# Kernel tuning notes

Measured on AMD Instinct MI355X. Metric: run time of the kernel, lower is better.

## Reference

```python
import jax, jax.numpy as jnp
import numpy as np

DIM = 256
NUM_HEADS = 8
HEAD_DIM = DIM // NUM_HEADS
NUM_MAIN = 2
NUM_MOD = 4
SEQ_MAIN = 1536
SEQ_AUX = 768
BS = 2


def setup_inputs() -> dict:
    key = jax.random.key(0)
    ks = jax.random.split(key, 6)
    x0 = jax.random.normal(ks[0], (BS, SEQ_MAIN, DIM), jnp.float32)
    x1 = jax.random.normal(ks[1], (BS, SEQ_MAIN, DIM), jnp.float32)
    x2 = jax.random.normal(ks[2], (BS, SEQ_AUX, DIM), jnp.float32)
    x3 = jax.random.normal(ks[3], (BS, SEQ_AUX, DIM), jnp.float32)
    Wqkv = jax.random.normal(ks[4], (NUM_MOD, DIM, 3 * DIM), jnp.float32) * 0.02
    bqkv = jnp.zeros((NUM_MOD, 3 * DIM), jnp.float32)
    Wproj = jax.random.normal(ks[5], (NUM_MOD, DIM, DIM), jnp.float32) * 0.02
    bproj = jnp.zeros((NUM_MOD, DIM), jnp.float32)
    return {"x0": x0, "x1": x1, "x2": x2, "x3": x3,
            "Wqkv": Wqkv, "bqkv": bqkv, "Wproj": Wproj, "bproj": bproj}


def _split_qkv(qkv):
    bs, s, _ = qkv.shape
    qkv = qkv.reshape(bs, s, 3, NUM_HEADS, HEAD_DIM).transpose(2, 0, 3, 1, 4)
    return qkv[0], qkv[1], qkv[2]


def _sdpa(q, k, v):
    scale = 1.0 / jnp.sqrt(jnp.asarray(HEAD_DIM, q.dtype))
    scores = jnp.einsum('bhqd,bhkd->bhqk', q, k) * scale
    probs = jax.nn.softmax(scores, axis=-1)
    return jnp.einsum('bhqk,bhkd->bhqd', probs, v)


def _merge_heads(t):
    # [bs, heads, s, head_dim] -> [bs, s, dim]
    bs, h, s, d = t.shape
    return t.transpose(0, 2, 1, 3).reshape(bs, s, h * d)


def reference(x0, x1, x2, x3, Wqkv, bqkv, Wproj, bproj):
    xs = [x0, x1, x2, x3]
    seqlens = [x.shape[1] for x in xs]
    qs, ks, vs = [], [], []
    for i in range(NUM_MOD):
        q, k, v = _split_qkv(xs[i] @ Wqkv[i] + bqkv[i])
        qs.append(q); ks.append(k); vs.append(v)

    main_q = jnp.concatenate(qs[:NUM_MAIN], axis=2)
    main_k = jnp.concatenate(ks[:NUM_MAIN], axis=2)
    main_v = jnp.concatenate(vs[:NUM_MAIN], axis=2)
    main_x = _merge_heads(_sdpa(main_q, main_k, main_v))  # [bs, sum(main seqlens), dim]
    splits = np.cumsum(seqlens[:NUM_MAIN])[:-1]
    outs = list(jnp.split(main_x, splits, axis=1))

    # aux modalities attend over detached main KV + own KV
    mk = jax.lax.stop_gradient(main_k)
    mv = jax.lax.stop_gradient(main_v)
    for i in range(NUM_MAIN, NUM_MOD):
        k = jnp.concatenate([mk, ks[i]], axis=2)
        v = jnp.concatenate([mv, vs[i]], axis=2)
        outs.append(_merge_heads(_sdpa(qs[i], k, v)))

    outs = [outs[i] @ Wproj[i] + bproj[i] for i in range(NUM_MOD)]
    # concatenate per-modality outputs along the sequence dim for a single output
    return jnp.concatenate(outs, axis=1)
```

## Files before the change

### kernel.cpp

```cpp
#include <hip/hip_runtime.h>
#include <hip/hip_bf16.h>
#include <math.h>

#define BS 2
#define NHEADS 8
#define HD 32
#define DIM 256
#define W3 768
#define S_MAIN 1536
#define S_AUX 768
#define SM_TOT 3072
#define S_TOT 4608

typedef _Float16 f16x8 __attribute__((ext_vector_type(8)));
typedef _Float16 f16x4 __attribute__((ext_vector_type(4)));
typedef float    f32x4 __attribute__((ext_vector_type(4)));

#define QK_SCALE 0.25503491f

#define QM_H  0
#define KM_H  1572864
#define VMT_H 3145728
#define QA_H  4718592
#define KA_H  5505024
#define VAT_H 6291456
#define AO0_F 3538944
#define AO1_F 5898240
#define L0_F  8257536
#define L1_F  8266752

#define GLOAD_LDS(SRC, DST)                                                    \
    __builtin_amdgcn_global_load_lds(                                          \
        (const __attribute__((address_space(1))) void*)(SRC),                  \
        (__attribute__((address_space(3))) void*)(DST), 16, 0, 0)

__global__ __launch_bounds__(256) void qkv_mfma_kernel(
    const float* __restrict__ x0, const float* __restrict__ x1,
    const float* __restrict__ x2, const float* __restrict__ x3,
    const float* __restrict__ Wqkv, const float* __restrict__ bqkv,
    _Float16* __restrict__ wsh)
{
    const int m  = blockIdx.z;
    const int rt = blockIdx.y;
    const int ct = blockIdx.x;
    const int s_m   = (m < 2) ? S_MAIN : S_AUX;
    const int nrows = BS * s_m;
    const int r0 = rt * 128;
    if (r0 >= nrows) return;

    const float* x    = (m == 0) ? x0 : (m == 1) ? x1 : (m == 2) ? x2 : x3;
    const float* W    = Wqkv + m * (DIM * W3);
    const float* bias = bqkv + m * W3;

    __shared__ _Float16 As[128][40];
    __shared__ _Float16 Bs[64][40];

    const int t    = threadIdx.x;
    const int wid  = t >> 6;
    const int lane = t & 63;
    const int g    = lane >> 4;
    const int c    = lane & 15;
    const int c0   = ct * 64;

    const int arow = t >> 1;
    const int ak   = (t & 1) << 4;
    const int bcol = t & 63;
    const int bkg  = t >> 6;
    const int bsg  = bkg ^ ((bcol >> 3) & 3);

    f32x4 acc[2][4];
    #pragma unroll
    for (int i = 0; i < 2; ++i)
        #pragma unroll
        for (int j = 0; j < 4; ++j)
            acc[i][j] = (f32x4){0.f, 0.f, 0.f, 0.f};

    const float* xp = x + (r0 + arow) * DIM + ak;
    const float* wp = W + (bkg * 8) * W3 + c0 + bcol;

    for (int kk = 0; kk < DIM; kk += 32) {
        {
            const float4 u0 = *(const float4*)(xp + kk + 0);
            const float4 u1 = *(const float4*)(xp + kk + 4);
            const float4 u2 = *(const float4*)(xp + kk + 8);
            const float4 u3 = *(const float4*)(xp + kk + 12);
            f16x8 h0, h1;
            h0[0] = (_Float16)u0.x; h0[1] = (_Float16)u0.y;
            h0[2] = (_Float16)u0.z; h0[3] = (_Float16)u0.w;
            h0[4] = (_Float16)u1.x; h0[5] = (_Float16)u1.y;
            h0[6] = (_Float16)u1.z; h0[7] = (_Float16)u1.w;
            h1[0] = (_Float16)u2.x; h1[1] = (_Float16)u2.y;
            h1[2] = (_Float16)u2.z; h1[3] = (_Float16)u2.w;
            h1[4] = (_Float16)u3.x; h1[5] = (_Float16)u3.y;
            h1[6] = (_Float16)u3.z; h1[7] = (_Float16)u3.w;
            *(f16x8*)&As[arow][ak]     = h0;
            *(f16x8*)&As[arow][ak + 8] = h1;
        }
        {
            const float* wq = wp + kk * W3;
            f16x8 hb;
            hb[0] = (_Float16)wq[0 * W3]; hb[1] = (_Float16)wq[1 * W3];
            hb[2] = (_Float16)wq[2 * W3]; hb[3] = (_Float16)wq[3 * W3];
            hb[4] = (_Float16)wq[4 * W3]; hb[5] = (_Float16)wq[5 * W3];
            hb[6] = (_Float16)wq[6 * W3]; hb[7] = (_Float16)wq[7 * W3];
            *(f16x8*)&Bs[bcol][bsg << 3] = hb;
        }
        __syncthreads();
        const f16x8 af0 = *(const f16x8*)&As[wid * 32 + c][g * 8];
        const f16x8 af1 = *(const f16x8*)&As[wid * 32 + 16 + c][g * 8];
        #pragma unroll
        for (int j = 0; j < 4; ++j) {
            const int bc = j * 16 + c;
            const int gg = g ^ ((bc >> 3) & 3);
            const f16x8 bf = *(const f16x8*)&Bs[bc][gg * 8];
            acc[0][j] = __builtin_amdgcn_mfma_f32_16x16x32_f16(af0, bf, acc[0][j], 0, 0, 0);
            acc[1][j] = __builtin_amdgcn_mfma_f32_16x16x32_f16(af1, bf, acc[1][j], 0, 0, 0);
        }
        __syncthreads();
    }

    #pragma unroll
    for (int i = 0; i < 2; ++i) {
        const int gr = r0 + wid * 32 + i * 16 + 4 * g;
        const int b  = (gr >= s_m) ? 1 : 0;
        const int s  = gr - (b ? s_m : 0);
        #pragma unroll
        for (int j = 0; j < 4; ++j) {
            const int col   = c0 + j * 16 + c;
            const int which = col >> 8;
            const int head  = (col >> 5) & 7;
            const int dd    = col & 31;
            const float bv  = bias[col];
            const f32x4 a   = acc[i][j];
            if (which < 2) {
                const float qs = (which == 0) ? QK_SCALE : 1.0f;
                _Float16* dst;
                int base;
                if (m < 2) {
                    dst  = wsh + (which == 0 ? QM_H : KM_H);
                    base = ((b * NHEADS + head) * SM_TOT + (s + m * S_MAIN)) * HD + dd;
                } else {
                    dst  = wsh + (which == 0 ? QA_H : KA_H);
                    base = ((((m - 2) * BS + b) * NHEADS + head) * S_AUX + s) * HD + dd;
                }
                dst[base + 0 * HD] = (_Float16)((a[0] + bv) * qs);
                dst[base + 1 * HD] = (_Float16)((a[1] + bv) * qs);
                dst[base + 2 * HD] = (_Float16)((a[2] + bv) * qs);
                dst[base + 3 * HD] = (_Float16)((a[3] + bv) * qs);
            } else {
                _Float16* dst;
                int base;
                if (m < 2) {
                    dst  = wsh + VMT_H;
                    base = ((b * NHEADS + head) * HD + dd) * SM_TOT + (s + m * S_MAIN);
                } else {
                    dst  = wsh + VAT_H;
                    base = ((((m - 2) * BS + b) * NHEADS + head) * HD + dd) * S_AUX + s;
                }
                f16x4 hv;
                hv[0] = (_Float16)(a[0] + bv);
                hv[1] = (_Float16)(a[1] + bv);
                hv[2] = (_Float16)(a[2] + bv);
                hv[3] = (_Float16)(a[3] + bv);
                *(f16x4*)(dst + base) = hv;
            }
        }
    }
}

__global__ __launch_bounds__(256) void attn_mfma_kernel(
    const _Float16* __restrict__ wsh, float* __restrict__ wsf)
{
    __shared__ _Float16 kbuf[2][2][64 * 32];
    __shared__ _Float16 vbuf[2][2][32 * 64];

    const int wid  = threadIdx.x >> 6;
    const int lane = threadIdx.x & 63;
    const int g    = lane >> 4;
    const int c    = lane & 15;

    const int bid = blockIdx.x;

    const _Float16 *qp, *kp0, *vt0, *kp1, *vt1;
    int n0, n1, vs1, orow0, ocol, half;

    if (bid < 384) {
        const int mbhg = bid / 12;
        const int mod  = mbhg >> 4;
        const int b    = (mbhg >> 3) & 1;
        const int h    = mbhg & 7;
        const int t    = bid % 12;
        const int qt   = t >> 1;
        half = t & 1;
        const int q0   = qt * 128 + wid * 32;
        const int mbh  = (mod * BS + b) * NHEADS + h;
        const int bh   = b * NHEADS + h;
        qp = wsh + QA_H + (mbh * S_AUX + q0) * HD;
        if (half == 0) {
            kp0 = wsh + KM_H  + bh * SM_TOT * HD;
            vt0 = wsh + VMT_H + bh * HD * SM_TOT;
            n0  = 1920;
            kp1 = nullptr; vt1 = nullptr; n1 = 0; vs1 = 0;
        } else {
            kp0 = wsh + KM_H  + (bh * SM_TOT + 1920) * HD;
            vt0 = wsh + VMT_H + bh * HD * SM_TOT + 1920;
            n0  = 1152;
            kp1 = wsh + KA_H  + mbh * S_AUX * HD;
            vt1 = wsh + VAT_H + mbh * HD * S_AUX;
            n1  = S_AUX; vs1 = S_AUX;
        }
        orow0 = b * S_TOT + SM_TOT + mod * S_AUX + q0;
        ocol  = h * HD;
    } else {
        const int idx = bid - 384;
        const int bh  = idx / 48;
        const int t   = idx % 48;
        const int qt  = t >> 1;
        half = t & 1;
        const int q0  = qt * 128 + wid * 32;
        const int b = bh >> 3, h = bh & 7;
        const int ks = half * 1536;
        qp  = wsh + QM_H  + (bh * SM_TOT + q0) * HD;
        kp0 = wsh + KM_H  + (bh * SM_TOT + ks) * HD;
        vt0 = wsh + VMT_H + bh * HD * SM_TOT + ks;
        n0  = 1536;
        kp1 = nullptr; vt1 = nullptr; n1 = 0; vs1 = 0;
        orow0 = b * S_TOT + q0;
        ocol  = h * HD;
    }

    const f16x8 qfA = *(const f16x8*)(qp + c * HD + g * 8);
    const f16x8 qfB = *(const f16x8*)(qp + (16 + c) * HD + g * 8);

    const int pc    = ((c >> 2) << 3) + (c & 3);
    const int kchr  = (g ^ (c >> 2)) << 3;
    const int koff0 = pc * HD + kchr;
    const int koff1 = (pc + 4) * HD + kchr;

    const int krow  = wid * 16 + (lane >> 2);
    const int kchg  = ((lane & 3) ^ ((krow >> 3) & 3)) << 3;

    const int srow = wid * 8 + (lane >> 3);
    const int jl   = lane & 7;
    const int vswz = (jl ^ (srow & 7)) << 3;
    const int vr0 = ((g     ^ (c & 7)) << 3);
    const int vr1 = (((g+4) ^ (c & 7)) << 3);

    f16x8 ones;
    #pragma unroll
    for (int i = 0; i < 8; ++i) ones[i] = (_Float16)1.0f;

    f32x4 otA0 = {0.f, 0.f, 0.f, 0.f}, otA1 = {0.f, 0.f, 0.f, 0.f};
    f32x4 otB0 = {0.f, 0.f, 0.f, 0.f}, otB1 = {0.f, 0.f, 0.f, 0.f};
    f32x4 ltA  = {0.f, 0.f, 0.f, 0.f}, ltB  = {0.f, 0.f, 0.f, 0.f};

    int cur = 0;

    #pragma unroll 1
    for (int seg = 0; seg < 2; ++seg) {
        const _Float16* kp_ = seg ? kp1 : kp0;
        const _Float16* vt_ = seg ? vt1 : vt0;
        const int n  = seg ? n1  : n0;
        const int vs = seg ? vs1 : SM_TOT;
        if (n == 0) break;

        #define STAGE(BI, S, K0)                                               \
            {                                                                  \
                const _Float16* ks_ = kp_ + (K0 + krow) * HD + kchg;           \
                GLOAD_LDS(ks_, &kbuf[BI][S][wid * 512]);                       \
                const _Float16* vs_ = vt_ + (K0) + srow * vs + vswz;           \
                GLOAD_LDS(vs_, &vbuf[BI][S][wid * 512]);                       \
            }

        #define COMPUTE_TILE(BI, S)                                            \
            {                                                                  \
                const _Float16* kb_ = &kbuf[BI][S][0];                         \
                const _Float16* vb_ = &vbuf[BI][S][0];                         \
                const f16x8 kf0 = *(const f16x8*)(kb_ + koff0);                \
                const f16x8 kf1 = *(const f16x8*)(kb_ + koff1);                \
                const f16x8 kf2 = *(const f16x8*)(kb_ + 32 * HD + koff0);      \
                const f16x8 kf3 = *(const f16x8*)(kb_ + 32 * HD + koff1);      \
                const f16x8 va0 = *(const f16x8*)(vb_ + c * 64 + vr0);         \
                const f16x8 va1 = *(const f16x8*)(vb_ + (16 + c) * 64 + vr0);  \
                const f16x8 vb0 = *(const f16x8*)(vb_ + c * 64 + vr1);         \
                const f16x8 vb1 = *(const f16x8*)(vb_ + (16 + c) * 64 + vr1);  \
                f32x4 sA0 = __builtin_amdgcn_mfma_f32_16x16x32_f16(            \
                    kf0, qfA, (f32x4){0.f, 0.f, 0.f, 0.f}, 0, 0, 0);           \
                f32x4 sA1 = __builtin_amdgcn_mfma_f32_16x16x32_f16(            \
                    kf1, qfA, (f32x4){0.f, 0.f, 0.f, 0.f}, 0, 0, 0);           \
                f32x4 sA2 = __builtin_amdgcn_mfma_f32_16x16x32_f16(            \
                    kf2, qfA, (f32x4){0.f, 0.f, 0.f, 0.f}, 0, 0, 0);           \
                f32x4 sA3 = __builtin_amdgcn_mfma_f32_16x16x32_f16(            \
                    kf3, qfA, (f32x4){0.f, 0.f, 0.f, 0.f}, 0, 0, 0);           \
                f32x4 sB0 = __builtin_amdgcn_mfma_f32_16x16x32_f16(            \
                    kf0, qfB, (f32x4){0.f, 0.f, 0.f, 0.f}, 0, 0, 0);           \
                f32x4 sB1 = __builtin_amdgcn_mfma_f32_16x16x32_f16(            \
                    kf1, qfB, (f32x4){0.f, 0.f, 0.f, 0.f}, 0, 0, 0);           \
                f32x4 sB2 = __builtin_amdgcn_mfma_f32_16x16x32_f16(            \
                    kf2, qfB, (f32x4){0.f, 0.f, 0.f, 0.f}, 0, 0, 0);           \
                f32x4 sB3 = __builtin_amdgcn_mfma_f32_16x16x32_f16(            \
                    kf3, qfB, (f32x4){0.f, 0.f, 0.f, 0.f}, 0, 0, 0);           \
                float pA0[4], pA1[4], pA2[4], pA3[4];                          \
                float pB0[4], pB1[4], pB2[4], pB3[4];                          \
                _Pragma("unroll")                                              \
                for (int r = 0; r < 4; ++r) {                                  \
                    pA0[r] = __builtin_amdgcn_exp2f(sA0[r]);                   \
                    pA1[r] = __builtin_amdgcn_exp2f(sA1[r]);                   \
                    pA2[r] = __builtin_amdgcn_exp2f(sA2[r]);                   \
                    pA3[r] = __builtin_amdgcn_exp2f(sA3[r]);                   \
                    pB0[r] = __builtin_amdgcn_exp2f(sB0[r]);                   \
                    pB1[r] = __builtin_amdgcn_exp2f(sB1[r]);                   \
                    pB2[r] = __builtin_amdgcn_exp2f(sB2[r]);                   \
                    pB3[r] = __builtin_amdgcn_exp2f(sB3[r]);                   \
                }                                                              \
                f16x8 pbA0, pbA1, pbB0, pbB1;                                  \
                _Pragma("unroll")                                              \
                for (int r = 0; r < 4; ++r) {                                  \
                    pbA0[r]     = (_Float16)pA0[r];                            \
                    pbA0[r + 4] = (_Float16)pA1[r];                            \
                    pbA1[r]     = (_Float16)pA2[r];                            \
                    pbA1[r + 4] = (_Float16)pA3[r];                            \
                    pbB0[r]     = (_Float16)pB0[r];                            \
                    pbB0[r + 4] = (_Float16)pB1[r];                            \
                    pbB1[r]     = (_Float16)pB2[r];                            \
                    pbB1[r + 4] = (_Float16)pB3[r];                            \
                }                                                              \
                ltA = __builtin_amdgcn_mfma_f32_16x16x32_f16(ones, pbA0, ltA, 0, 0, 0); \
                ltA = __builtin_amdgcn_mfma_f32_16x16x32_f16(ones, pbA1, ltA, 0, 0, 0); \
                ltB = __builtin_amdgcn_mfma_f32_16x16x32_f16(ones, pbB0, ltB, 0, 0, 0); \
                ltB = __builtin_amdgcn_mfma_f32_16x16x32_f16(ones, pbB1, ltB, 0, 0, 0); \
                otA0 = __builtin_amdgcn_mfma_f32_16x16x32_f16(va0, pbA0, otA0, 0, 0, 0); \
                otA1 = __builtin_amdgcn_mfma_f32_16x16x32_f16(va1, pbA0, otA1, 0, 0, 0); \
                otB0 = __builtin_amdgcn_mfma_f32_16x16x32_f16(va0, pbB0, otB0, 0, 0, 0); \
                otB1 = __builtin_amdgcn_mfma_f32_16x16x32_f16(va1, pbB0, otB1, 0, 0, 0); \
                otA0 = __builtin_amdgcn_mfma_f32_16x16x32_f16(vb0, pbA1, otA0, 0, 0, 0); \
                otA1 = __builtin_amdgcn_mfma_f32_16x16x32_f16(vb1, pbA1, otA1, 0, 0, 0); \
                otB0 = __builtin_amdgcn_mfma_f32_16x16x32_f16(vb0, pbB1, otB0, 0, 0, 0); \
                otB1 = __builtin_amdgcn_mfma_f32_16x16x32_f16(vb1, pbB1, otB1, 0, 0, 0); \
            }

        STAGE(cur, 0, 0);
        STAGE(cur, 1, 64);
        __syncthreads();

        #pragma unroll 1
        for (int k0 = 0; k0 < n; k0 += 128) {
            if (k0 + 128 < n) {
                STAGE(cur ^ 1, 0, k0 + 128);
                STAGE(cur ^ 1, 1, k0 + 192);
            }
            COMPUTE_TILE(cur, 0);
            COMPUTE_TILE(cur, 1);
            __syncthreads();
            cur ^= 1;
        }

        #undef STAGE
        #undef COMPUTE_TILE
    }

    float* aoBase = wsf + (half ? AO1_F : AO0_F);
    float* lBase  = wsf + (half ? L1_F  : L0_F);

    float* aoA = aoBase + (orow0 + c) * DIM + ocol;
    float* aoB = aoBase + (orow0 + 16 + c) * DIM + ocol;
    float4 w0, w1, w2, w3;
    w0.x = otA0[0]; w0.y = otA0[1]; w0.z = otA0[2]; w0.w = otA0[3];
    w1.x = otA1[0]; w1.y = otA1[1]; w1.z = otA1[2]; w1.w = otA1[3];
    w2.x = otB0[0]; w2.y = otB0[1]; w2.z = otB0[2]; w2.w = otB0[3];
    w3.x = otB1[0]; w3.y = otB1[1]; w3.z = otB1[2]; w3.w = otB1[3];
    *(float4*)(aoA + 4 * g)      = w0;
    *(float4*)(aoA + 16 + 4 * g) = w1;
    *(float4*)(aoB + 4 * g)      = w2;
    *(float4*)(aoB + 16 + 4 * g) = w3;

    if (g == 0) {
        lBase[orow0 + c]      = ltA[0];
        lBase[orow0 + 16 + c] = ltB[0];
    }
}

__global__ __launch_bounds__(256) void proj_mfma_kernel(
    const float* __restrict__ wsf, const float* __restrict__ Wproj,
    const float* __restrict__ bproj, float* __restrict__ out)
{
    const int ct = blockIdx.x;
    const int rt = blockIdx.y;
    const int r0 = rt * 128, c0 = ct * 64;
    const int seq = r0 % S_TOT;
    const int mod = (seq < S_MAIN) ? 0 : (seq < SM_TOT) ? 1
                  : (seq < SM_TOT + S_AUX) ? 2 : 3;
    const float* W    = Wproj + mod * DIM * DIM;
    const float* bias = bproj + mod * DIM;
    const float* A0   = wsf + AO0_F;
    const float* A1   = wsf + AO1_F;
    const float* L0p  = wsf + L0_F;
    const float* L1p  = wsf + L1_F;

    __shared__ _Float16 As[128][40];
    __shared__ _Float16 Bs[64][40];
    __shared__ float Linv[128];

    const int t    = threadIdx.x;
    const int wid  = t >> 6;
    const int lane = t & 63;
    const int g    = lane >> 4;
    const int c    = lane & 15;

    if (t < 128) Linv[t] = 1.0f / (L0p[r0 + t] + L1p[r0 + t]);
    __syncthreads();

    const int arow = t >> 1;
    const int ak   = (t & 1) << 4;
    const int bcol = t & 63;
    const int bkg  = t >> 6;
    const int bsg  = bkg ^ ((bcol >> 3) & 3);
    const float linv_r = Linv[arow];

    f32x4 acc[2][4];
    #pragma unroll
    for (int i = 0; i < 2; ++i)
        #pragma unroll
        for (int j = 0; j < 4; ++j)
            acc[i][j] = (f32x4){0.f, 0.f, 0.f, 0.f};

    const float* pa0 = A0 + (r0 + arow) * DIM + ak;
    const float* pa1 = A1 + (r0 + arow) * DIM + ak;
    const float* wp  = W + (bkg * 8) * DIM + c0 + bcol;

    for (int kk = 0; kk < DIM; kk += 32) {
        {
            const float4 u0 = *(const float4*)(pa0 + kk + 0);
            const float4 u1 = *(const float4*)(pa0 + kk + 4);
            const float4 u2 = *(const float4*)(pa0 + kk + 8);
            const float4 u3 = *(const float4*)(pa0 + kk + 12);
            const float4 v0 = *(const float4*)(pa1 + kk + 0);
            const float4 v1 = *(const float4*)(pa1 + kk + 4);
            const float4 v2 = *(const float4*)(pa1 + kk + 8);
            const float4 v3 = *(const float4*)(pa1 + kk + 12);
            f16x8 h0, h1;
            h0[0] = (_Float16)((u0.x + v0.x) * linv_r);
            h0[1] = (_Float16)((u0.y + v0.y) * linv_r);
            h0[2] = (_Float16)((u0.z + v0.z) * linv_r);
            h0[3] = (_Float16)((u0.w + v0.w) * linv_r);
            h0[4] = (_Float16)((u1.x + v1.x) * linv_r);
            h0[5] = (_Float16)((u1.y + v1.y) * linv_r);
            h0[6] = (_Float16)((u1.z + v1.z) * linv_r);
            h0[7] = (_Float16)((u1.w + v1.w) * linv_r);
            h1[0] = (_Float16)((u2.x + v2.x) * linv_r);
            h1[1] = (_Float16)((u2.y + v2.y) * linv_r);
            h1[2] = (_Float16)((u2.z + v2.z) * linv_r);
            h1[3] = (_Float16)((u2.w + v2.w) * linv_r);
            h1[4] = (_Float16)((u3.x + v3.x) * linv_r);
            h1[5] = (_Float16)((u3.y + v3.y) * linv_r);
            h1[6] = (_Float16)((u3.z + v3.z) * linv_r);
            h1[7] = (_Float16)((u3.w + v3.w) * linv_r);
            *(f16x8*)&As[arow][ak]     = h0;
            *(f16x8*)&As[arow][ak + 8] = h1;
        }
        {
            const float* wq = wp + kk * DIM;
            f16x8 hb;
            hb[0] = (_Float16)wq[0 * DIM]; hb[1] = (_Float16)wq[1 * DIM];
            hb[2] = (_Float16)wq[2 * DIM]; hb[3] = (_Float16)wq[3 * DIM];
            hb[4] = (_Float16)wq[4 * DIM]; hb[5] = (_Float16)wq[5 * DIM];
            hb[6] = (_Float16)wq[6 * DIM]; hb[7] = (_Float16)wq[7 * DIM];
            *(f16x8*)&Bs[bcol][bsg << 3] = hb;
        }
        __syncthreads();
        const f16x8 af0 = *(const f16x8*)&As[wid * 32 + c][g * 8];
        const f16x8 af1 = *(const f16x8*)&As[wid * 32 + 16 + c][g * 8];
        #pragma unroll
        for (int j = 0; j < 4; ++j) {
            const int bc = j * 16 + c;
            const int gg = g ^ ((bc >> 3) & 3);
            const f16x8 bf = *(const f16x8*)&Bs[bc][gg * 8];
            acc[0][j] = __builtin_amdgcn_mfma_f32_16x16x32_f16(af0, bf, acc[0][j], 0, 0, 0);
            acc[1][j] = __builtin_amdgcn_mfma_f32_16x16x32_f16(af1, bf, acc[1][j], 0, 0, 0);
        }
        __syncthreads();
    }

    #pragma unroll
    for (int i = 0; i < 2; ++i) {
        const int gr = r0 + wid * 32 + i * 16 + 4 * g;
        #pragma unroll
        for (int j = 0; j < 4; ++j) {
            const int col  = c0 + j * 16 + c;
            const float bv = bias[col];
            const f32x4 a  = acc[i][j];
            out[(gr + 0) * DIM + col] = a[0] + bv;
            out[(gr + 1) * DIM + col] = a[1] + bv;
            out[(gr + 2) * DIM + col] = a[2] + bv;
            out[(gr + 3) * DIM + col] = a[3] + bv;
        }
    }
}

extern "C" void kernel_launch(void* const* d_in, const int* in_sizes, int n_in,
                              void* d_out, int out_size, void* d_ws, size_t ws_size,
                              hipStream_t stream)
{
    const float* x0    = (const float*)d_in[0];
    const float* x1    = (const float*)d_in[1];
    const float* x2    = (const float*)d_in[2];
    const float* x3    = (const float*)d_in[3];
    const float* Wqkv  = (const float*)d_in[4];
    const float* bqkv  = (const float*)d_in[5];
    const float* Wproj = (const float*)d_in[6];
    const float* bproj = (const float*)d_in[7];
    _Float16* wsh = (_Float16*)d_ws;
    float*    wsf = (float*)d_ws;
    float*    out = (float*)d_out;

    qkv_mfma_kernel<<<dim3(12, 24, 4), 256, 0, stream>>>(
        x0, x1, x2, x3, Wqkv, bqkv, wsh);

    attn_mfma_kernel<<<dim3(1152), 256, 0, stream>>>(wsh, wsf);

    proj_mfma_kernel<<<dim3(4, 72), 256, 0, stream>>>(wsf, Wproj, bproj, out);
}
```

Measured before the change: 91.95 us.

## Flatten attention segments into one 4-deep LDS ring with vmcnt-gated prefetch

Merges the two KV segments into a single loop over 64-key tiles and replaces the double-buffered 128-key stage with a four-slot LDS ring, prefetching two tiles ahead. Each iteration waits with explicit s_waitcnt vmcnt counts and a raw s_barrier instead of a full __syncthreads, so loads of later tiles can stay in flight during compute. This removes the per-segment pipeline drain and refill. The risk is correctness: only one barrier per tile, combined with a ring of four slots and a prefetch distance of two, must keep stores to slot t+2 from overwriting data that slower waves are still reading.

```diff
diff --git a/kernel.cpp b/kernel.cpp
--- a/kernel.cpp
+++ b/kernel.cpp
@@ -171,8 +171,8 @@
 __global__ __launch_bounds__(256) void attn_mfma_kernel(
     const _Float16* __restrict__ wsh, float* __restrict__ wsf)
 {
-    __shared__ _Float16 kbuf[2][2][64 * 32];
-    __shared__ _Float16 vbuf[2][2][32 * 64];
+    __shared__ _Float16 kbuf[4][64 * 32];
+    __shared__ _Float16 vbuf[4][32 * 64];
 
     const int wid  = threadIdx.x >> 6;
     const int lane = threadIdx.x & 63;
@@ -254,110 +254,107 @@
     f32x4 otB0 = {0.f, 0.f, 0.f, 0.f}, otB1 = {0.f, 0.f, 0.f, 0.f};
     f32x4 ltA  = {0.f, 0.f, 0.f, 0.f}, ltB  = {0.f, 0.f, 0.f, 0.f};
 
-    int cur = 0;
+    const int nt0  = n0 >> 6;
+    const int ntot = (n0 + n1) >> 6;
+
+    #define STAGE_T(T, BI)                                                     \
+        {                                                                      \
+            const _Float16* kp_; const _Float16* vt_; int vs_s, k0_;           \
+            if ((T) < nt0) { kp_ = kp0; vt_ = vt0; vs_s = SM_TOT; k0_ = (T) << 6; } \
+            else           { kp_ = kp1; vt_ = vt1; vs_s = vs1;   k0_ = ((T) - nt0) << 6; } \
+            const _Float16* ks_ = kp_ + (k0_ + krow) * HD + kchg;              \
+            GLOAD_LDS(ks_, &kbuf[BI][wid * 512]);                              \
+            const _Float16* vsp = vt_ + k0_ + srow * vs_s + vswz;              \
+            GLOAD_LDS(vsp, &vbuf[BI][wid * 512]);                              \
+        }
+
+    #define COMPUTE_TILE(BI)                                                   \
+        {                                                                      \
+            const _Float16* kb_ = &kbuf[BI][0];                                \
+            const _Float16* vb_ = &vbuf[BI][0];                                \
+            const f16x8 kf0 = *(const f16x8*)(kb_ + koff0);                    \
+            const f16x8 kf1 = *(const f16x8*)(kb_ + koff1);                    \
+            const f16x8 kf2 = *(const f16x8*)(kb_ + 32 * HD + koff0);          \
+            const f16x8 kf3 = *(const f16x8*)(kb_ + 32 * HD + koff1);          \
+            const f16x8 va0 = *(const f16x8*)(vb_ + c * 64 + vr0);             \
+            const f16x8 va1 = *(const f16x8*)(vb_ + (16 + c) * 64 + vr0);      \
+            const f16x8 vb0 = *(const f16x8*)(vb_ + c * 64 + vr1);             \
+            const f16x8 vb1 = *(const f16x8*)(vb_ + (16 + c) * 64 + vr1);      \
+            f32x4 sA0 = __builtin_amdgcn_mfma_f32_16x16x32_f16(                \
+                kf0, qfA, (f32x4){0.f, 0.f, 0.f, 0.f}, 0, 0, 0);               \
+            f32x4 sA1 = __builtin_amdgcn_mfma_f32_16x16x32_f16(                \
+                kf1, qfA, (f32x4){0.f, 0.f, 0.f, 0.f}, 0, 0, 0);               \
+            f32x4 sA2 = __builtin_amdgcn_mfma_f32_16x16x32_f16(                \
+                kf2, qfA, (f32x4){0.f, 0.f, 0.f, 0.f}, 0, 0, 0);               \
+            f32x4 sA3 = __builtin_amdgcn_mfma_f32_16x16x32_f16(                \
+                kf3, qfA, (f32x4){0.f, 0.f, 0.f, 0.f}, 0, 0, 0);               \
+            f32x4 sB0 = __builtin_amdgcn_mfma_f32_16x16x32_f16(                \
+                kf0, qfB, (f32x4){0.f, 0.f, 0.f, 0.f}, 0, 0, 0);               \
+            f32x4 sB1 = __builtin_amdgcn_mfma_f32_16x16x32_f16(                \
+                kf1, qfB, (f32x4){0.f, 0.f, 0.f, 0.f}, 0, 0, 0);               \
+            f32x4 sB2 = __builtin_amdgcn_mfma_f32_16x16x32_f16(                \
+                kf2, qfB, (f32x4){0.f, 0.f, 0.f, 0.f}, 0, 0, 0);               \
+            f32x4 sB3 = __builtin_amdgcn_mfma_f32_16x16x32_f16(                \
+                kf3, qfB, (f32x4){0.f, 0.f, 0.f, 0.f}, 0, 0, 0);               \
+            float pA0[4], pA1[4], pA2[4], pA3[4];                              \
+            float pB0[4], pB1[4], pB2[4], pB3[4];                              \
+            _Pragma("unroll")                                                  \
+            for (int r = 0; r < 4; ++r) {                                      \
+                pA0[r] = __builtin_amdgcn_exp2f(sA0[r]);                       \
+                pA1[r] = __builtin_amdgcn_exp2f(sA1[r]);                       \
+                pA2[r] = __builtin_amdgcn_exp2f(sA2[r]);                       \
+                pA3[r] = __builtin_amdgcn_exp2f(sA3[r]);                       \
+                pB0[r] = __builtin_amdgcn_exp2f(sB0[r]);                       \
+                pB1[r] = __builtin_amdgcn_exp2f(sB1[r]);                       \
+                pB2[r] = __builtin_amdgcn_exp2f(sB2[r]);                       \
+                pB3[r] = __builtin_amdgcn_exp2f(sB3[r]);                       \
+            }                                                                  \
+            f16x8 pbA0, pbA1, pbB0, pbB1;                                      \
+            _Pragma("unroll")                                                  \
+            for (int r = 0; r < 4; ++r) {                                      \
+                pbA0[r]     = (_Float16)pA0[r];                                \
+                pbA0[r + 4] = (_Float16)pA1[r];                                \
+                pbA1[r]     = (_Float16)pA2[r];                                \
+                pbA1[r + 4] = (_Float16)pA3[r];                                \
+                pbB0[r]     = (_Float16)pB0[r];                                \
+                pbB0[r + 4] = (_Float16)pB1[r];                                \
+                pbB1[r]     = (_Float16)pB2[r];                                \
+                pbB1[r + 4] = (_Float16)pB3[r];                                \
+            }                                                                  \
+            ltA = __builtin_amdgcn_mfma_f32_16x16x32_f16(ones, pbA0, ltA, 0, 0, 0); \
+            ltA = __builtin_amdgcn_mfma_f32_16x16x32_f16(ones, pbA1, ltA, 0, 0, 0); \
+            ltB = __builtin_amdgcn_mfma_f32_16x16x32_f16(ones, pbB0, ltB, 0, 0, 0); \
+            ltB = __builtin_amdgcn_mfma_f32_16x16x32_f16(ones, pbB1, ltB, 0, 0, 0); \
+            otA0 = __builtin_amdgcn_mfma_f32_16x16x32_f16(va0, pbA0, otA0, 0, 0, 0); \
+            otA1 = __builtin_amdgcn_mfma_f32_16x16x32_f16(va1, pbA0, otA1, 0, 0, 0); \
+            otB0 = __builtin_amdgcn_mfma_f32_16x16x32_f16(va0, pbB0, otB0, 0, 0, 0); \
+            otB1 = __builtin_amdgcn_mfma_f32_16x16x32_f16(va1, pbB0, otB1, 0, 0, 0); \
+            otA0 = __builtin_amdgcn_mfma_f32_16x16x32_f16(vb0, pbA1, otA0, 0, 0, 0); \
+            otA1 = __builtin_amdgcn_mfma_f32_16x16x32_f16(vb1, pbA1, otA1, 0, 0, 0); \
+            otB0 = __builtin_amdgcn_mfma_f32_16x16x32_f16(vb0, pbB1, otB0, 0, 0, 0); \
+            otB1 = __builtin_amdgcn_mfma_f32_16x16x32_f16(vb1, pbB1, otB1, 0, 0, 0); \
+        }
+
+    STAGE_T(0, 0);
+    STAGE_T(1, 1);
 
     #pragma unroll 1
-    for (int seg = 0; seg < 2; ++seg) {
-        const _Float16* kp_ = seg ? kp1 : kp0;
-        const _Float16* vt_ = seg ? vt1 : vt0;
-        const int n  = seg ? n1  : n0;
-        const int vs = seg ? vs1 : SM_TOT;
-        if (n == 0) break;
-
-        #define STAGE(BI, S, K0)                                               \
-            {                                                                  \
-                const _Float16* ks_ = kp_ + (K0 + krow) * HD + kchg;           \
-                GLOAD_LDS(ks_, &kbuf[BI][S][wid * 512]);                       \
-                const _Float16* vs_ = vt_ + (K0) + srow * vs + vswz;           \
-                GLOAD_LDS(vs_, &vbuf[BI][S][wid * 512]);                       \
-            }
-
-        #define COMPUTE_TILE(BI, S)                                            \
-            {                                                                  \
-                const _Float16* kb_ = &kbuf[BI][S][0];                         \
-                const _Float16* vb_ = &vbuf[BI][S][0];                         \
-                const f16x8 kf0 = *(const f16x8*)(kb_ + koff0);                \
-                const f16x8 kf1 = *(const f16x8*)(kb_ + koff1);                \
-                const f16x8 kf2 = *(const f16x8*)(kb_ + 32 * HD + koff0);      \
-                const f16x8 kf3 = *(const f16x8*)(kb_ + 32 * HD + koff1);      \
-                const f16x8 va0 = *(const f16x8*)(vb_ + c * 64 + vr0);         \
-                const f16x8 va1 = *(const f16x8*)(vb_ + (16 + c) * 64 + vr0);  \
-                const f16x8 vb0 = *(const f16x8*)(vb_ + c * 64 + vr1);         \
-                const f16x8 vb1 = *(const f16x8*)(vb_ + (16 + c) * 64 + vr1);  \
-                f32x4 sA0 = __builtin_amdgcn_mfma_f32_16x16x32_f16(            \
-                    kf0, qfA, (f32x4){0.f, 0.f, 0.f, 0.f}, 0, 0, 0);           \
-                f32x4 sA1 = __builtin_amdgcn_mfma_f32_16x16x32_f16(            \
-                    kf1, qfA, (f32x4){0.f, 0.f, 0.f, 0.f}, 0, 0, 0);           \
-                f32x4 sA2 = __builtin_amdgcn_mfma_f32_16x16x32_f16(            \
-                    kf2, qfA, (f32x4){0.f, 0.f, 0.f, 0.f}, 0, 0, 0);           \
-                f32x4 sA3 = __builtin_amdgcn_mfma_f32_16x16x32_f16(            \
-                    kf3, qfA, (f32x4){0.f, 0.f, 0.f, 0.f}, 0, 0, 0);           \
-                f32x4 sB0 = __builtin_amdgcn_mfma_f32_16x16x32_f16(            \
-                    kf0, qfB, (f32x4){0.f, 0.f, 0.f, 0.f}, 0, 0, 0);           \
-                f32x4 sB1 = __builtin_amdgcn_mfma_f32_16x16x32_f16(            \
-                    kf1, qfB, (f32x4){0.f, 0.f, 0.f, 0.f}, 0, 0, 0);           \
-                f32x4 sB2 = __builtin_amdgcn_mfma_f32_16x16x32_f16(            \
-                    kf2, qfB, (f32x4){0.f, 0.f, 0.f, 0.f}, 0, 0, 0);           \
-                f32x4 sB3 = __builtin_amdgcn_mfma_f32_16x16x32_f16(            \
-                    kf3, qfB, (f32x4){0.f, 0.f, 0.f, 0.f}, 0, 0, 0);           \
-                float pA0[4], pA1[4], pA2[4], pA3[4];                          \
-                float pB0[4], pB1[4], pB2[4], pB3[4];                          \
-                _Pragma("unroll")                                              \
-                for (int r = 0; r < 4; ++r) {                                  \
-                    pA0[r] = __builtin_amdgcn_exp2f(sA0[r]);                   \
-                    pA1[r] = __builtin_amdgcn_exp2f(sA1[r]);                   \
-                    pA2[r] = __builtin_amdgcn_exp2f(sA2[r]);                   \
-                    pA3[r] = __builtin_amdgcn_exp2f(sA3[r]);                   \
-                    pB0[r] = __builtin_amdgcn_exp2f(sB0[r]);                   \
-                    pB1[r] = __builtin_amdgcn_exp2f(sB1[r]);                   \
-                    pB2[r] = __builtin_amdgcn_exp2f(sB2[r]);                   \
-                    pB3[r] = __builtin_amdgcn_exp2f(sB3[r]);                   \
-                }                                                              \
-                f16x8 pbA0, pbA1, pbB0, pbB1;                                  \
-                _Pragma("unroll")                                              \
-                for (int r = 0; r < 4; ++r) {                                  \
-                    pbA0[r]     = (_Float16)pA0[r];                            \
-                    pbA0[r + 4] = (_Float16)pA1[r];                            \
-                    pbA1[r]     = (_Float16)pA2[r];                            \
-                    pbA1[r + 4] = (_Float16)pA3[r];                            \
-                    pbB0[r]     = (_Float16)pB0[r];                            \
-                    pbB0[r + 4] = (_Float16)pB1[r];                            \
-                    pbB1[r]     = (_Float16)pB2[r];                            \
-                    pbB1[r + 4] = (_Float16)pB3[r];                            \
-                }                                                              \
-                ltA = __builtin_amdgcn_mfma_f32_16x16x32_f16(ones, pbA0, ltA, 0, 0, 0); \
-                ltA = __builtin_amdgcn_mfma_f32_16x16x32_f16(ones, pbA1, ltA, 0, 0, 0); \
-                ltB = __builtin_amdgcn_mfma_f32_16x16x32_f16(ones, pbB0, ltB, 0, 0, 0); \
-                ltB = __builtin_amdgcn_mfma_f32_16x16x32_f16(ones, pbB1, ltB, 0, 0, 0); \
-                otA0 = __builtin_amdgcn_mfma_f32_16x16x32_f16(va0, pbA0, otA0, 0, 0, 0); \
-                otA1 = __builtin_amdgcn_mfma_f32_16x16x32_f16(va1, pbA0, otA1, 0, 0, 0); \
-                otB0 = __builtin_amdgcn_mfma_f32_16x16x32_f16(va0, pbB0, otB0, 0, 0, 0); \
-                otB1 = __builtin_amdgcn_mfma_f32_16x16x32_f16(va1, pbB0, otB1, 0, 0, 0); \
-                otA0 = __builtin_amdgcn_mfma_f32_16x16x32_f16(vb0, pbA1, otA0, 0, 0, 0); \
-                otA1 = __builtin_amdgcn_mfma_f32_16x16x32_f16(vb1, pbA1, otA1, 0, 0, 0); \
-                otB0 = __builtin_amdgcn_mfma_f32_16x16x32_f16(vb0, pbB1, otB0, 0, 0, 0); \
-                otB1 = __builtin_amdgcn_mfma_f32_16x16x32_f16(vb1, pbB1, otB1, 0, 0, 0); \
-            }
-
-        STAGE(cur, 0, 0);
-        STAGE(cur, 1, 64);
-        __syncthreads();
-
-        #pragma unroll 1
-        for (int k0 = 0; k0 < n; k0 += 128) {
-            if (k0 + 128 < n) {
-                STAGE(cur ^ 1, 0, k0 + 128);
-                STAGE(cur ^ 1, 1, k0 + 192);
-            }
-            COMPUTE_TILE(cur, 0);
-            COMPUTE_TILE(cur, 1);
-            __syncthreads();
-            cur ^= 1;
-        }
-
-        #undef STAGE
-        #undef COMPUTE_TILE
-    }
+    for (int t = 0; t < ntot; ++t) {
+        if (t + 2 < ntot) {
+            STAGE_T(t + 2, (t + 2) & 3);
+            asm volatile("s_waitcnt vmcnt(4)" ::: "memory");
+        } else if (t + 1 < ntot) {
+            asm volatile("s_waitcnt vmcnt(2)" ::: "memory");
+        } else {
+            asm volatile("s_waitcnt vmcnt(0)" ::: "memory");
+        }
+        __builtin_amdgcn_s_barrier();
+        __builtin_amdgcn_sched_barrier(0);
+        COMPUTE_TILE(t & 3);
+    }
+
+    #undef STAGE_T
+    #undef COMPUTE_TILE
 
     float* aoBase = wsf + (half ? AO1_F : AO0_F);
     float* lBase  = wsf + (half ? L1_F  : L0_F);
```

Result: no change. 93.23 us (+1.4%).

## Double per-wave query rows in attention to halve K/V tile reloads

Applied to the files above, without the earlier changes.

Each wave now processes 64 query rows (four 16-row fragments) instead of 32, so each block covers 256 queries and the grid shrinks from 1152 to 576 blocks. Every K/V tile staged in LDS and read into registers is reused across twice as many queries, which halves global K/V traffic and LDS fragment reads per unit of work. The cost is more accumulator registers per wave, possibly lower occupancy, and fewer blocks to spread across the 256 CUs (576 blocks is about 2.25 waves' worth, which leaves a tail).

```diff
diff --git a/kernel.cpp b/kernel.cpp
--- a/kernel.cpp
+++ b/kernel.cpp
@@ -184,15 +184,15 @@
     const _Float16 *qp, *kp0, *vt0, *kp1, *vt1;
     int n0, n1, vs1, orow0, ocol, half;
 
-    if (bid < 384) {
-        const int mbhg = bid / 12;
+    if (bid < 192) {
+        const int mbhg = bid / 6;
         const int mod  = mbhg >> 4;
         const int b    = (mbhg >> 3) & 1;
         const int h    = mbhg & 7;
-        const int t    = bid % 12;
+        const int t    = bid % 6;
         const int qt   = t >> 1;
         half = t & 1;
-        const int q0   = qt * 128 + wid * 32;
+        const int q0   = qt * 256 + wid * 64;
         const int mbh  = (mod * BS + b) * NHEADS + h;
         const int bh   = b * NHEADS + h;
         qp = wsh + QA_H + (mbh * S_AUX + q0) * HD;
@@ -212,12 +212,12 @@
         orow0 = b * S_TOT + SM_TOT + mod * S_AUX + q0;
         ocol  = h * HD;
     } else {
-        const int idx = bid - 384;
-        const int bh  = idx / 48;
-        const int t   = idx % 48;
+        const int idx = bid - 192;
+        const int bh  = idx / 24;
+        const int t   = idx % 24;
         const int qt  = t >> 1;
         half = t & 1;
-        const int q0  = qt * 128 + wid * 32;
+        const int q0  = qt * 256 + wid * 64;
         const int b = bh >> 3, h = bh & 7;
         const int ks = half * 1536;
         qp  = wsh + QM_H  + (bh * SM_TOT + q0) * HD;
@@ -229,8 +229,10 @@
         ocol  = h * HD;
     }
 
-    const f16x8 qfA = *(const f16x8*)(qp + c * HD + g * 8);
+    const f16x8 qfA = *(const f16x8*)(qp + (     c) * HD + g * 8);
     const f16x8 qfB = *(const f16x8*)(qp + (16 + c) * HD + g * 8);
+    const f16x8 qfC = *(const f16x8*)(qp + (32 + c) * HD + g * 8);
+    const f16x8 qfD = *(const f16x8*)(qp + (48 + c) * HD + g * 8);
 
     const int pc    = ((c >> 2) << 3) + (c & 3);
     const int kchr  = (g ^ (c >> 2)) << 3;
@@ -250,9 +252,12 @@
     #pragma unroll
     for (int i = 0; i < 8; ++i) ones[i] = (_Float16)1.0f;
 
-    f32x4 otA0 = {0.f, 0.f, 0.f, 0.f}, otA1 = {0.f, 0.f, 0.f, 0.f};
-    f32x4 otB0 = {0.f, 0.f, 0.f, 0.f}, otB1 = {0.f, 0.f, 0.f, 0.f};
-    f32x4 ltA  = {0.f, 0.f, 0.f, 0.f}, ltB  = {0.f, 0.f, 0.f, 0.f};
+    f32x4 otA0 = {0.f,0.f,0.f,0.f}, otA1 = {0.f,0.f,0.f,0.f};
+    f32x4 otB0 = {0.f,0.f,0.f,0.f}, otB1 = {0.f,0.f,0.f,0.f};
+    f32x4 otC0 = {0.f,0.f,0.f,0.f}, otC1 = {0.f,0.f,0.f,0.f};
+    f32x4 otD0 = {0.f,0.f,0.f,0.f}, otD1 = {0.f,0.f,0.f,0.f};
+    f32x4 ltA  = {0.f,0.f,0.f,0.f}, ltB  = {0.f,0.f,0.f,0.f};
+    f32x4 ltC  = {0.f,0.f,0.f,0.f}, ltD  = {0.f,0.f,0.f,0.f};
 
     int cur = 0;
 
@@ -270,6 +275,40 @@
                 GLOAD_LDS(ks_, &kbuf[BI][S][wid * 512]);                       \
                 const _Float16* vs_ = vt_ + (K0) + srow * vs + vswz;           \
                 GLOAD_LDS(vs_, &vbuf[BI][S][wid * 512]);                       \
+            }
+
+        #define QBODY(QF, OT0, OT1, LT)                                        \
+            {                                                                  \
+                f32x4 s0 = __builtin_amdgcn_mfma_f32_16x16x32_f16(             \
+                    kf0, QF, (f32x4){0.f, 0.f, 0.f, 0.f}, 0, 0, 0);            \
+                f32x4 s1 = __builtin_amdgcn_mfma_f32_16x16x32_f16(             \
+                    kf1, QF, (f32x4){0.f, 0.f, 0.f, 0.f}, 0, 0, 0);            \
+                f32x4 s2 = __builtin_amdgcn_mfma_f32_16x16x32_f16(             \
+                    kf2, QF, (f32x4){0.f, 0.f, 0.f, 0.f}, 0, 0, 0);            \
+                f32x4 s3 = __builtin_amdgcn_mfma_f32_16x16x32_f16(             \
+                    kf3, QF, (f32x4){0.f, 0.f, 0.f, 0.f}, 0, 0, 0);            \
+                float p0[4], p1[4], p2[4], p3[4];                              \
+                _Pragma("unroll")                                              \
+                for (int r = 0; r < 4; ++r) {                                  \
+                    p0[r] = __builtin_amdgcn_exp2f(s0[r]);                     \
+                    p1[r] = __builtin_amdgcn_exp2f(s1[r]);                     \
+                    p2[r] = __builtin_amdgcn_exp2f(s2[r]);                     \
+                    p3[r] = __builtin_amdgcn_exp2f(s3[r]);                     \
+                }                                                              \
+                f16x8 pb0, pb1;                                                \
+                _Pragma("unroll")                                              \
+                for (int r = 0; r < 4; ++r) {                                  \
+                    pb0[r]     = (_Float16)p0[r];                              \
+                    pb0[r + 4] = (_Float16)p1[r];                              \
+                    pb1[r]     = (_Float16)p2[r];                              \
+                    pb1[r + 4] = (_Float16)p3[r];                              \
+                }                                                              \
+                LT  = __builtin_amdgcn_mfma_f32_16x16x32_f16(ones, pb0, LT, 0, 0, 0);  \
+                LT  = __builtin_amdgcn_mfma_f32_16x16x32_f16(ones, pb1, LT, 0, 0, 0);  \
+                OT0 = __builtin_amdgcn_mfma_f32_16x16x32_f16(va0, pb0, OT0, 0, 0, 0);  \
+                OT1 = __builtin_amdgcn_mfma_f32_16x16x32_f16(va1, pb0, OT1, 0, 0, 0);  \
+                OT0 = __builtin_amdgcn_mfma_f32_16x16x32_f16(vb0, pb1, OT0, 0, 0, 0);  \
+                OT1 = __builtin_amdgcn_mfma_f32_16x16x32_f16(vb1, pb1, OT1, 0, 0, 0);  \
             }
 
         #define COMPUTE_TILE(BI, S)                                            \
@@ -284,59 +323,10 @@
                 const f16x8 va1 = *(const f16x8*)(vb_ + (16 + c) * 64 + vr0);  \
                 const f16x8 vb0 = *(const f16x8*)(vb_ + c * 64 + vr1);         \
                 const f16x8 vb1 = *(const f16x8*)(vb_ + (16 + c) * 64 + vr1);  \
-                f32x4 sA0 = __builtin_amdgcn_mfma_f32_16x16x32_f16(            \
-                    kf0, qfA, (f32x4){0.f, 0.f, 0.f, 0.f}, 0, 0, 0);           \
-                f32x4 sA1 = __builtin_amdgcn_mfma_f32_16x16x32_f16(            \
-                    kf1, qfA, (f32x4){0.f, 0.f, 0.f, 0.f}, 0, 0, 0);           \
-                f32x4 sA2 = __builtin_amdgcn_mfma_f32_16x16x32_f16(            \
-                    kf2, qfA, (f32x4){0.f, 0.f, 0.f, 0.f}, 0, 0, 0);           \
-                f32x4 sA3 = __builtin_amdgcn_mfma_f32_16x16x32_f16(            \
-                    kf3, qfA, (f32x4){0.f, 0.f, 0.f, 0.f}, 0, 0, 0);           \
-                f32x4 sB0 = __builtin_amdgcn_mfma_f32_16x16x32_f16(            \
-                    kf0, qfB, (f32x4){0.f, 0.f, 0.f, 0.f}, 0, 0, 0);           \
-                f32x4 sB1 = __builtin_amdgcn_mfma_f32_16x16x32_f16(            \
-                    kf1, qfB, (f32x4){0.f, 0.f, 0.f, 0.f}, 0, 0, 0);           \
-                f32x4 sB2 = __builtin_amdgcn_mfma_f32_16x16x32_f16(            \
-                    kf2, qfB, (f32x4){0.f, 0.f, 0.f, 0.f}, 0, 0, 0);           \
-                f32x4 sB3 = __builtin_amdgcn_mfma_f32_16x16x32_f16(            \
-                    kf3, qfB, (f32x4){0.f, 0.f, 0.f, 0.f}, 0, 0, 0);           \
-                float pA0[4], pA1[4], pA2[4], pA3[4];                          \
-                float pB0[4], pB1[4], pB2[4], pB3[4];                          \
-                _Pragma("unroll")                                              \
-                for (int r = 0; r < 4; ++r) {                                  \
-                    pA0[r] = __builtin_amdgcn_exp2f(sA0[r]);                   \
-                    pA1[r] = __builtin_amdgcn_exp2f(sA1[r]);                   \
-                    pA2[r] = __builtin_amdgcn_exp2f(sA2[r]);                   \
-                    pA3[r] = __builtin_amdgcn_exp2f(sA3[r]);                   \
-                    pB0[r] = __builtin_amdgcn_exp2f(sB0[r]);                   \
-                    pB1[r] = __builtin_amdgcn_exp2f(sB1[r]);                   \
-                    pB2[r] = __builtin_amdgcn_exp2f(sB2[r]);                   \
-                    pB3[r] = __builtin_amdgcn_exp2f(sB3[r]);                   \
-                }                                                              \
-                f16x8 pbA0, pbA1, pbB0, pbB1;                                  \
-                _Pragma("unroll")                                              \
-                for (int r = 0; r < 4; ++r) {                                  \
-                    pbA0[r]     = (_Float16)pA0[r];                            \
-                    pbA0[r + 4] = (_Float16)pA1[r];                            \
-                    pbA1[r]     = (_Float16)pA2[r];                            \
-                    pbA1[r + 4] = (_Float16)pA3[r];                            \
-                    pbB0[r]     = (_Float16)pB0[r];                            \
-                    pbB0[r + 4] = (_Float16)pB1[r];                            \
-                    pbB1[r]     = (_Float16)pB2[r];                            \
-                    pbB1[r + 4] = (_Float16)pB3[r];                            \
-                }                                                              \
-                ltA = __builtin_amdgcn_mfma_f32_16x16x32_f16(ones, pbA0, ltA, 0, 0, 0); \
-                ltA = __builtin_amdgcn_mfma_f32_16x16x32_f16(ones, pbA1, ltA, 0, 0, 0); \
-                ltB = __builtin_amdgcn_mfma_f32_16x16x32_f16(ones, pbB0, ltB, 0, 0, 0); \
-                ltB = __builtin_amdgcn_mfma_f32_16x16x32_f16(ones, pbB1, ltB, 0, 0, 0); \
-                otA0 = __builtin_amdgcn_mfma_f32_16x16x32_f16(va0, pbA0, otA0, 0, 0, 0); \
-                otA1 = __builtin_amdgcn_mfma_f32_16x16x32_f16(va1, pbA0, otA1, 0, 0, 0); \
-                otB0 = __builtin_amdgcn_mfma_f32_16x16x32_f16(va0, pbB0, otB0, 0, 0, 0); \
-                otB1 = __builtin_amdgcn_mfma_f32_16x16x32_f16(va1, pbB0, otB1, 0, 0, 0); \
-                otA0 = __builtin_amdgcn_mfma_f32_16x16x32_f16(vb0, pbA1, otA0, 0, 0, 0); \
-                otA1 = __builtin_amdgcn_mfma_f32_16x16x32_f16(vb1, pbA1, otA1, 0, 0, 0); \
-                otB0 = __builtin_amdgcn_mfma_f32_16x16x32_f16(vb0, pbB1, otB0, 0, 0, 0); \
-                otB1 = __builtin_amdgcn_mfma_f32_16x16x32_f16(vb1, pbB1, otB1, 0, 0, 0); \
+                QBODY(qfA, otA0, otA1, ltA)                                    \
+                QBODY(qfB, otB0, otB1, ltB)                                    \
+                QBODY(qfC, otC0, otC1, ltC)                                    \
+                QBODY(qfD, otD0, otD1, ltD)                                    \
             }
 
         STAGE(cur, 0, 0);
@@ -356,28 +346,29 @@
         }
 
         #undef STAGE
+        #undef QBODY
         #undef COMPUTE_TILE
     }
 
     float* aoBase = wsf + (half ? AO1_F : AO0_F);
     float* lBase  = wsf + (half ? L1_F  : L0_F);
 
-    float* aoA = aoBase + (orow0 + c) * DIM + ocol;
-    float* aoB = aoBase + (orow0 + 16 + c) * DIM + ocol;
-    float4 w0, w1, w2, w3;
-    w0.x = otA0[0]; w0.y = otA0[1]; w0.z = otA0[2]; w0.w = otA0[3];
-    w1.x = otA1[0]; w1.y = otA1[1]; w1.z = otA1[2]; w1.w = otA1[3];
-    w2.x = otB0[0]; w2.y = otB0[1]; w2.z = otB0[2]; w2.w = otB0[3];
-    w3.x = otB1[0]; w3.y = otB1[1]; w3.z = otB1[2]; w3.w = otB1[3];
-    *(float4*)(aoA + 4 * g)      = w0;
-    *(float4*)(aoA + 16 + 4 * g) = w1;
-    *(float4*)(aoB + 4 * g)      = w2;
-    *(float4*)(aoB + 16 + 4 * g) = w3;
-
-    if (g == 0) {
-        lBase[orow0 + c]      = ltA[0];
-        lBase[orow0 + 16 + c] = ltB[0];
-    }
+    #define STORE_Q(F, OT0, OT1, LT)                                           \
+        {                                                                      \
+            float* ao = aoBase + (orow0 + (F) * 16 + c) * DIM + ocol;          \
+            float4 w0, w1;                                                     \
+            w0.x = OT0[0]; w0.y = OT0[1]; w0.z = OT0[2]; w0.w = OT0[3];        \
+            w1.x = OT1[0]; w1.y = OT1[1]; w1.z = OT1[2]; w1.w = OT1[3];        \
+            *(float4*)(ao + 4 * g)      = w0;                                  \
+            *(float4*)(ao + 16 + 4 * g) = w1;                                  \
+            if (g == 0) lBase[orow0 + (F) * 16 + c] = LT[0];                   \
+        }
+
+    STORE_Q(0, otA0, otA1, ltA)
+    STORE_Q(1, otB0, otB1, ltB)
+    STORE_Q(2, otC0, otC1, ltC)
+    STORE_Q(3, otD0, otD1, ltD)
+    #undef STORE_Q
 }
 
 __global__ __launch_bounds__(256) void proj_mfma_kernel(
@@ -516,7 +507,7 @@
     qkv_mfma_kernel<<<dim3(12, 24, 4), 256, 0, stream>>>(
         x0, x1, x2, x3, Wqkv, bqkv, wsh);
 
-    attn_mfma_kernel<<<dim3(1152), 256, 0, stream>>>(wsh, wsf);
+    attn_mfma_kernel<<<dim3(576), 256, 0, stream>>>(wsh, wsf);
 
     proj_mfma_kernel<<<dim3(4, 72), 256, 0, stream>>>(wsf, Wproj, bproj, out);
 }
```

Result: slower. 97.43 us (+6.0%).
